# Performance work log

Measured on AMD Instinct MI355X. Metric: run time of the kernel, lower is better.

## Reference

```python
import jax, jax.numpy as jnp
import numpy as np

EMBED_DIM = 1024
NUM_HEADS = 16
HEAD_DIM = EMBED_DIM // NUM_HEADS


def setup_inputs() -> dict:
    key = jax.random.key(0)
    ks = jax.random.split(key, 9)
    B, T, D = 2, 4096, EMBED_DIM
    scale = 1.0 / np.sqrt(D)
    x = jax.random.normal(ks[0], (B, T, D), dtype=jnp.float32)
    # nn.Linear weights stored as (out, in); we use (in, out) layout via transpose-free init
    Wq = jax.random.uniform(ks[1], (D, D), dtype=jnp.float32, minval=-scale, maxval=scale)
    Wk = jax.random.uniform(ks[2], (D, D), dtype=jnp.float32, minval=-scale, maxval=scale)
    Wv = jax.random.uniform(ks[3], (D, D), dtype=jnp.float32, minval=-scale, maxval=scale)
    Wo = jax.random.uniform(ks[4], (D, D), dtype=jnp.float32, minval=-scale, maxval=scale)
    bq = jax.random.uniform(ks[5], (D,), dtype=jnp.float32, minval=-scale, maxval=scale)
    bk = jax.random.uniform(ks[6], (D,), dtype=jnp.float32, minval=-scale, maxval=scale)
    bv = jax.random.uniform(ks[7], (D,), dtype=jnp.float32, minval=-scale, maxval=scale)
    bo = jax.random.uniform(ks[8], (D,), dtype=jnp.float32, minval=-scale, maxval=scale)
    return {"x": x, "Wq": Wq, "bq": bq, "Wk": Wk, "bk": bk,
            "Wv": Wv, "bv": bv, "Wo": Wo, "bo": bo}


def reference(x, Wq, bq, Wk, bk, Wv, bv, Wo, bo):
    B, T, D = x.shape
    H, Hd = NUM_HEADS, HEAD_DIM
    q = x @ Wq + bq  # [B,T,D]
    k = x @ Wk + bk
    v = x @ Wv + bv
    # [B,T,D] -> [B,H,T,Hd]
    q = q.reshape(B, T, H, Hd).transpose(0, 2, 1, 3)
    k = k.reshape(B, T, H, Hd).transpose(0, 2, 1, 3)
    v = v.reshape(B, T, H, Hd).transpose(0, 2, 1, 3)
    att = jnp.einsum('bhqd,bhkd->bhqk', q, k) / jnp.sqrt(jnp.float32(Hd))
    causal = jnp.tril(jnp.ones((T, T), dtype=bool))  # True = keep
    att = jnp.where(causal, att, -jnp.inf)
    att = jax.nn.softmax(att, axis=-1)
    out = jnp.einsum('bhqk,bhkd->bhqd', att, v)  # [B,H,T,Hd]
    out = out.transpose(0, 2, 1, 3).reshape(B, T, D)
    return out @ Wo + bo
```

## Files before the change

### kernel.cpp

```cpp
#include <hip/hip_runtime.h>
#include <hip/hip_bf16.h>
#include <math.h>

typedef __bf16 bf16;
typedef __attribute__((ext_vector_type(8))) __bf16 bf16x8;
typedef __attribute__((ext_vector_type(4))) __bf16 bf16x4;
typedef __attribute__((ext_vector_type(4))) short short4v;
typedef __attribute__((ext_vector_type(4))) float f32x4;

#define MFMA16(a,b,c)  __builtin_amdgcn_mfma_f32_16x16x32_bf16((a),(b),(c),0,0,0)
#define MFMAK16(a,b,c) __builtin_amdgcn_mfma_f32_16x16x16bf16_1k((a),(b),(c),0,0,0)

__device__ __forceinline__ void gload16(const void* gp, void* lp) {
  __builtin_amdgcn_global_load_lds(
      (const __attribute__((address_space(1))) void*)gp,
      (__attribute__((address_space(3))) void*)lp, 16, 0, 0);
}

__global__ __launch_bounds__(256) void cast_x(
    const float* __restrict__ x, bf16* __restrict__ xb)
{
  size_t i = ((size_t)blockIdx.x*256 + threadIdx.x) * 8;
  f32x4 a = *(const f32x4*)(x+i);
  f32x4 b = *(const f32x4*)(x+i+4);
  bf16x8 o;
  #pragma unroll
  for (int j=0;j<4;j++) { o[j] = (bf16)a[j]; o[4+j] = (bf16)b[j]; }
  *(bf16x8*)(xb+i) = o;
}

__global__ __launch_bounds__(1024) void tr_cast(
    const float* __restrict__ w0, const float* __restrict__ w1,
    const float* __restrict__ w2, bf16* __restrict__ dst)
{
  __shared__ bf16 tile[64][65];
  const float* src = (blockIdx.z==0)?w0:(blockIdx.z==1)?w1:w2;
  bf16* d = dst + (size_t)blockIdx.z * (1024*1024);
  int x = threadIdx.x, y = threadIdx.y;
  int tc = blockIdx.x, tr = blockIdx.y;
  #pragma unroll
  for (int i=0;i<4;i++) {
    int r = y + i*16;
    tile[r][x] = (bf16)src[(size_t)(tr*64+r)*1024 + tc*64 + x];
  }
  __syncthreads();
  #pragma unroll
  for (int i=0;i<4;i++) {
    int r = y + i*16;
    d[(size_t)(tc*64+r)*1024 + tr*64 + x] = tile[x][r];
  }
}

__global__ __launch_bounds__(1024) void v_tr(
    const bf16* __restrict__ v, bf16* __restrict__ vt)
{
  __shared__ bf16 tile[64][65];
  int x = threadIdx.x, y = threadIdx.y;
  int tt = blockIdx.x;
  int bh = blockIdx.y;
  int b = bh >> 4, h = bh & 15;
  const bf16* src = v + ((size_t)b*4096 + tt*64)*1024 + h*64;
  bf16* dst = vt + ((size_t)bh*64)*4096 + tt*64;
  #pragma unroll
  for (int i=0;i<4;i++) {
    int r = y + i*16;
    tile[r][x] = src[(size_t)r*1024 + x];
  }
  __syncthreads();
  #pragma unroll
  for (int i=0;i<4;i++) {
    int r = y + i*16;
    dst[(size_t)r*4096 + x] = tile[x][r];
  }
}

__global__ __launch_bounds__(256) void gemm_qkv(
    const bf16* __restrict__ A, const bf16* __restrict__ Bt,
    const float* __restrict__ bq, const float* __restrict__ bk, const float* __restrict__ bv,
    bf16* __restrict__ q, bf16* __restrict__ k, bf16* __restrict__ v,
    int M, int K)
{
  __shared__ __align__(16) bf16 As[128*64];
  __shared__ __align__(16) bf16 Bs[128*64];
  const int tid  = threadIdx.x;
  const int wave = tid >> 6;
  const int lane = tid & 63;
  const int l15  = lane & 15;
  const int quad = lane >> 4;

  const int wg  = blockIdx.x + blockIdx.y*24;
  const int nid = (wg & 7)*192 + (wg >> 3);
  const int m0 = (nid / 24) * 128;
  const int n0 = (nid % 24) * 128;

  const int wm = (wave >> 1) * 64;
  const int wn = (wave & 1) * 64;

  int srow[4], scol[4];
  #pragma unroll
  for (int p=0;p<4;p++) {
    int cid = p*256 + tid;
    srow[p] = cid >> 3;
    scol[p] = ((cid & 7) ^ (srow[p] & 7)) << 3;
  }
  const int swz8 = l15 & 7;
  int rdo[2];
  #pragma unroll
  for (int kk=0;kk<2;kk++) rdo[kk] = (((kk*4 + quad) ^ swz8) << 3);

  f32x4 acc[4][4];
  #pragma unroll
  for (int i=0;i<4;i++)
    #pragma unroll
    for (int j=0;j<4;j++)
      acc[i][j] = (f32x4){0.f,0.f,0.f,0.f};

  for (int k0 = 0; k0 < K; k0 += 64) {
    __syncthreads();
    #pragma unroll
    for (int p=0;p<4;p++) {
      int cid = p*256 + tid;
      gload16(A  + (size_t)(m0+srow[p])*K + k0 + scol[p], As + cid*8);
      gload16(Bt + (size_t)(n0+srow[p])*K + k0 + scol[p], Bs + cid*8);
    }
    __syncthreads();
    #pragma unroll
    for (int kk=0;kk<2;kk++) {
      bf16x8 af[4], bfr[4];
      #pragma unroll
      for (int t=0;t<4;t++) {
        af[t]  = *(const bf16x8*)(As + (wm + t*16 + l15)*64 + rdo[kk]);
        bfr[t] = *(const bf16x8*)(Bs + (wn + t*16 + l15)*64 + rdo[kk]);
      }
      #pragma unroll
      for (int mt=0;mt<4;mt++)
        #pragma unroll
        for (int nt=0;nt<4;nt++)
          acc[mt][nt] = MFMA16(af[mt], bfr[nt], acc[mt][nt]);
    }
  }

  const int mat = n0 >> 10;
  const float* bsel = (mat==0) ? bq : (mat==1) ? bk : bv;
  bf16*       osel  = (mat==0) ? q  : (mat==1) ? k  : v;
  const float qsc   = (mat==0) ? 0.1803368801f : 1.0f;
  #pragma unroll
  for (int nt=0;nt<4;nt++) {
    int col = n0 + wn + nt*16 + l15;
    int cw  = col & 1023;
    float bvv = bsel[cw];
    #pragma unroll
    for (int mt=0;mt<4;mt++) {
      int row = m0 + wm + mt*16 + quad*4;
      #pragma unroll
      for (int r=0;r<4;r++)
        osel[(size_t)(row + r)*1024 + cw] = (bf16)((acc[mt][nt][r] + bvv) * qsc);
    }
  }
}

__global__ __launch_bounds__(256, 4) void gemm_out(
    const bf16* __restrict__ A, const bf16* __restrict__ Bt,
    const float* __restrict__ bias, float* __restrict__ C,
    int M, int N, int K)
{
  __shared__ __align__(16) bf16 As[128*64];
  __shared__ __align__(16) bf16 Bs[64*64];
  const int tid  = threadIdx.x;
  const int wave = tid >> 6;
  const int lane = tid & 63;
  const int l15  = lane & 15;
  const int quad = lane >> 4;

  const int wg  = blockIdx.x + blockIdx.y*16;
  const int nid = (wg & 7)*128 + (wg >> 3);
  const int m0 = (nid / 16) * 128;
  const int n0 = (nid % 16) * 64;

  const int wm = (wave >> 1) * 64;
  const int wn = (wave & 1) * 32;

  int srow[4], scol[4];
  #pragma unroll
  for (int p=0;p<4;p++) {
    int cid = p*256 + tid;
    srow[p] = cid >> 3;
    scol[p] = ((cid & 7) ^ (srow[p] & 7)) << 3;
  }
  const int swz8 = l15 & 7;
  int rdo[2];
  #pragma unroll
  for (int kk=0;kk<2;kk++) rdo[kk] = (((kk*4 + quad) ^ swz8) << 3);

  f32x4 acc[4][2];
  #pragma unroll
  for (int i=0;i<4;i++)
    #pragma unroll
    for (int j=0;j<2;j++)
      acc[i][j] = (f32x4){0.f,0.f,0.f,0.f};

  for (int k0 = 0; k0 < K; k0 += 64) {
    __syncthreads();
    #pragma unroll
    for (int p=0;p<4;p++)
      gload16(A + (size_t)(m0+srow[p])*K + k0 + scol[p], As + (p*256+tid)*8);
    #pragma unroll
    for (int p=0;p<2;p++) {
      int cid = p*256 + tid;
      gload16(Bt + (size_t)(n0+srow[p])*K + k0 + scol[p], Bs + cid*8);
    }
    __syncthreads();
    #pragma unroll
    for (int kk=0;kk<2;kk++) {
      bf16x8 af[4], bfr[2];
      #pragma unroll
      for (int t=0;t<4;t++)
        af[t]  = *(const bf16x8*)(As + (wm + t*16 + l15)*64 + rdo[kk]);
      #pragma unroll
      for (int t=0;t<2;t++)
        bfr[t] = *(const bf16x8*)(Bs + (wn + t*16 + l15)*64 + rdo[kk]);
      #pragma unroll
      for (int mt=0;mt<4;mt++)
        #pragma unroll
        for (int nt=0;nt<2;nt++)
          acc[mt][nt] = MFMA16(af[mt], bfr[nt], acc[mt][nt]);
    }
  }

  #pragma unroll
  for (int nt=0;nt<2;nt++) {
    int col = n0 + wn + nt*16 + l15;
    float bvv = bias[col];
    #pragma unroll
    for (int mt=0;mt<4;mt++) {
      int row = m0 + wm + mt*16 + quad*4;
      #pragma unroll
      for (int r=0;r<4;r++)
        C[(size_t)(row + r)*N + col] = acc[mt][nt][r] + bvv;
    }
  }
}

__global__ __launch_bounds__(256, 2) void attn_fwd(
    const bf16* __restrict__ Q, const bf16* __restrict__ Kp,
    const bf16* __restrict__ Vtg, bf16* __restrict__ O)
{
  __shared__ __align__(16) char KsB[4*8192];
  __shared__ __align__(16) char VtB[4*8192];

  const int tid  = threadIdx.x;
  const int w    = tid >> 6;
  const int lane = tid & 63;
  const int l15  = lane & 15;
  const int quad = lane >> 4;

  const int bid = blockIdx.x;
  const int pp  = bid >> 5;
  const int bh  = bid & 31;
  const int h   = bh & 15;
  const int b   = bh >> 4;

  const size_t headoff = (size_t)h * 64;
  const size_t bbase   = (size_t)b * 4096;

  short4v ones_s;
  {
    bf16x4 o1;
    #pragma unroll
    for (int j=0;j<4;j++) o1[j] = (bf16)1.0f;
    ones_s = __builtin_bit_cast(short4v, o1);
  }

  const int kt_row = tid >> 2;
  const int kswz   = (kt_row & 7) << 4;
  const int ks_w0  = kt_row*128 + (((tid & 3)*32)      ^ kswz);
  const int ks_w1  = kt_row*128 + (((tid & 3)*32 + 16) ^ kswz);

  const int vd  = tid >> 2;
  const int vt0 = (tid & 3) * 16;
  int vw[4];
  #pragma unroll
  for (int u=0;u<4;u++)
    vw[u] = vd*128 + (((vt0 + u*4)*2) ^ ((vd & 15) << 3));

  const int s7    = l15 & 7;
  const int ks_r0 = l15*128 + ((quad ^ (s7 & 3)) << 4) + ((s7 >> 2) << 6);
  const int ks_r1 = ks_r0 ^ 64;
  const int vt_rbase = l15*128 + ((quad ^ (l15 & 3)) << 3) + ((l15 >> 2) << 5);
  int vt_r[4];
  #pragma unroll
  for (int tt=0;tt<4;tt++) vt_r[tt] = vt_rbase ^ (tt << 5);

  const bf16* kbase0 = Kp  + (bbase + kt_row)*1024 + headoff + (tid & 3)*16;
  const bf16* vbase0 = Vtg + ((size_t)(bh*64) + vd)*4096 + vt0;

  for (int ph = 0; ph < 2; ++ph) {
    const int qt = ph ? (31 - pp) : pp;
    const int q0 = qt * 128;
    const int ktmax = 2*qt + 1;

    bf16x8 aqA[2], aqB[2];
    {
      int rowA = q0 + w*16 + l15;
      const bf16* qp = Q + (bbase + rowA)*1024 + headoff + quad*8;
      aqA[0] = *(const bf16x8*)(qp);
      aqA[1] = *(const bf16x8*)(qp + 32);
      qp += 64*1024;
      aqB[0] = *(const bf16x8*)(qp);
      aqB[1] = *(const bf16x8*)(qp + 32);
    }

    f32x4 accoA[4], accoB[4], accliA, accliB;
    #pragma unroll
    for (int i=0;i<4;i++) { accoA[i] = (f32x4){0.f,0.f,0.f,0.f}; accoB[i] = (f32x4){0.f,0.f,0.f,0.f}; }
    accliA = (f32x4){0.f,0.f,0.f,0.f};
    accliB = (f32x4){0.f,0.f,0.f,0.f};

    __syncthreads();
    #pragma unroll
    for (int j=0;j<2;j++) {
      const bf16* kp = kbase0 + (size_t)j*64*1024;
      const bf16* vp = vbase0 + j*64;
      bf16x8 k0 = *(const bf16x8*)(kp);
      bf16x8 k1 = *(const bf16x8*)(kp + 8);
      bf16x8 v0 = *(const bf16x8*)(vp);
      bf16x8 v1 = *(const bf16x8*)(vp + 8);
      char* ksn = KsB + j*8192;
      char* vtn = VtB + j*8192;
      *(bf16x8*)(ksn + ks_w0) = k0;
      *(bf16x8*)(ksn + ks_w1) = k1;
      *(bf16x4*)(vtn + vw[0]) = __builtin_shufflevector(v0, v0, 0,1,2,3);
      *(bf16x4*)(vtn + vw[1]) = __builtin_shufflevector(v0, v0, 4,5,6,7);
      *(bf16x4*)(vtn + vw[2]) = __builtin_shufflevector(v1, v1, 0,1,2,3);
      *(bf16x4*)(vtn + vw[3]) = __builtin_shufflevector(v1, v1, 4,5,6,7);
    }
    __syncthreads();

    const bf16* kpref = kbase0 + (size_t)2*64*1024;
    const bf16* vpref = vbase0 + 128;

    for (int kt = 0; kt <= ktmax; ++kt) {
      const bool pre = (kt + 2 <= ktmax);

      bf16x8 kr0, kr1, vr0, vr1;
      if (pre) {
        kr0 = *(const bf16x8*)(kpref);
        kr1 = *(const bf16x8*)(kpref + 8);
        vr0 = *(const bf16x8*)(vpref);
        vr1 = *(const bf16x8*)(vpref + 8);
        kpref += 64*1024;
        vpref += 64;
      }

      const char* ksb = KsB + (kt & 3)*8192;
      const char* vtb = VtB + (kt & 3)*8192;

      f32x4 accsA[4], accsB[4];
      #pragma unroll
      for (int i=0;i<4;i++) { accsA[i] = (f32x4){0.f,0.f,0.f,0.f}; accsB[i] = (f32x4){0.f,0.f,0.f,0.f}; }

      __builtin_amdgcn_s_setprio(1);
      #pragma unroll
      for (int kk=0;kk<2;kk++) {
        #pragma unroll
        for (int tt=0;tt<4;tt++) {
          bf16x8 ka = *(const bf16x8*)(ksb + (kk ? ks_r1 : ks_r0) + tt*2048);
          accsA[tt] = MFMA16(ka, aqA[kk], accsA[tt]);
          accsB[tt] = MFMA16(ka, aqB[kk], accsB[tt]);
        }
      }
      __builtin_amdgcn_s_setprio(0);

      short4v ptsA[4], ptsB[4];
      if (kt < 2*qt) {
        #pragma unroll
        for (int tt=0;tt<4;tt++) {
          bf16x4 pa, pb;
          #pragma unroll
          for (int r=0;r<4;r++) {
            pa[r] = (bf16)__builtin_amdgcn_exp2f(accsA[tt][r]);
            pb[r] = (bf16)__builtin_amdgcn_exp2f(accsB[tt][r]);
          }
          ptsA[tt] = __builtin_bit_cast(short4v, pa);
          ptsB[tt] = __builtin_bit_cast(short4v, pb);
        }
      } else {
        const bool adead = (kt > 2*qt);
        #pragma unroll
        for (int tt=0;tt<4;tt++) {
          bf16x4 pa, pb;
          #pragma unroll
          for (int r=0;r<4;r++) {
            const bool tq = (tt*16 + quad*4 + r > w*16 + l15);
            float fa = __builtin_amdgcn_exp2f(accsA[tt][r]);
            if (adead || tq) fa = 0.0f;
            float fb = __builtin_amdgcn_exp2f(accsB[tt][r]);
            if (adead && tq) fb = 0.0f;
            pa[r] = (bf16)fa; pb[r] = (bf16)fb;
          }
          ptsA[tt] = __builtin_bit_cast(short4v, pa);
          ptsB[tt] = __builtin_bit_cast(short4v, pb);
        }
      }

      __builtin_amdgcn_s_setprio(1);
      #pragma unroll
      for (int nt=0;nt<4;nt++) {
        #pragma unroll
        for (int tt=0;tt<4;tt++) {
          bf16x4 va = *(const bf16x4*)(vtb + vt_r[tt] + nt*2048);
          short4v vas = __builtin_bit_cast(short4v, va);
          accoA[nt] = MFMAK16(vas, ptsA[tt], accoA[nt]);
          accoB[nt] = MFMAK16(vas, ptsB[tt], accoB[nt]);
        }
      }
      #pragma unroll
      for (int tt=0;tt<4;tt++) {
        accliA = MFMAK16(ones_s, ptsA[tt], accliA);
        accliB = MFMAK16(ones_s, ptsB[tt], accliB);
      }
      __builtin_amdgcn_s_setprio(0);

      if (pre) {
        char* ksn = KsB + ((kt + 2) & 3)*8192;
        char* vtn = VtB + ((kt + 2) & 3)*8192;
        *(bf16x8*)(ksn + ks_w0) = kr0;
        *(bf16x8*)(ksn + ks_w1) = kr1;
        *(bf16x4*)(vtn + vw[0]) = __builtin_shufflevector(vr0, vr0, 0,1,2,3);
        *(bf16x4*)(vtn + vw[1]) = __builtin_shufflevector(vr0, vr0, 4,5,6,7);
        *(bf16x4*)(vtn + vw[2]) = __builtin_shufflevector(vr1, vr1, 0,1,2,3);
        *(bf16x4*)(vtn + vw[3]) = __builtin_shufflevector(vr1, vr1, 4,5,6,7);
      }
      if (kt & 1) __syncthreads();
    }

    {
      float invA = 1.0f / accliA[0];
      float invB = 1.0f / accliB[0];
      int rowA = q0 + w*16 + l15;
      bf16* obA = O + (bbase + rowA)*1024 + headoff;
      bf16* obB = obA + 64*1024;
      #pragma unroll
      for (int nt=0;nt<4;nt++) {
        bf16x4 oA, oB;
        #pragma unroll
        for (int r=0;r<4;r++) {
          oA[r] = (bf16)(accoA[nt][r] * invA);
          oB[r] = (bf16)(accoB[nt][r] * invB);
        }
        *(bf16x4*)(obA + nt*16 + quad*4) = oA;
        *(bf16x4*)(obB + nt*16 + quad*4) = oB;
      }
    }
  }
}

extern "C" void kernel_launch(void* const* d_in, const int* in_sizes, int n_in,
                              void* d_out, int out_size, void* d_ws, size_t ws_size,
                              hipStream_t stream) {
  const float* x  = (const float*)d_in[0];
  const float* Wq = (const float*)d_in[1];
  const float* bq = (const float*)d_in[2];
  const float* Wk = (const float*)d_in[3];
  const float* bk = (const float*)d_in[4];
  const float* Wv = (const float*)d_in[5];
  const float* bv = (const float*)d_in[6];
  const float* Wo = (const float*)d_in[7];
  const float* bo = (const float*)d_in[8];
  float* out = (float*)d_out;

  bf16* ws = (bf16*)d_ws;
  bf16* q  = ws;
  bf16* k  = q + (size_t)8192*1024;
  bf16* v  = k + (size_t)8192*1024;
  bf16* xb = v + (size_t)8192*1024;
  bf16* ao = q;
  bf16* WtQKV = (bf16*)d_out;
  bf16* vT    = (bf16*)d_out;
  bf16* WtO   = xb;

  tr_cast<<<dim3(16,16,3), dim3(64,16), 0, stream>>>(Wq, Wk, Wv, WtQKV);
  cast_x<<<4096, 256, 0, stream>>>(x, xb);
  gemm_qkv<<<dim3(24,64), 256, 0, stream>>>(xb, WtQKV, bq, bk, bv, q, k, v, 8192, 1024);
  v_tr<<<dim3(64,32), dim3(64,16), 0, stream>>>(v, vT);
  tr_cast<<<dim3(16,16,1), dim3(64,16), 0, stream>>>(Wo, Wo, Wo, WtO);
  attn_fwd<<<512, 256, 0, stream>>>(q, k, vT, ao);
  gemm_out<<<dim3(16,64), 256, 0, stream>>>(ao, WtO, bo, out, 8192, 1024, 1024);
}
```

Before: 296.2 us.

## Software-pipeline QK^T of next key tile with softmax/PV of current tile

Restructures the attention inner loop so the QK^T MFMAs for key tile kt+1 are issued before the exp/mask and PV work of tile kt. Two ping-pong score accumulator sets are used, and a macro unrolls the loop by two. The aim is to overlap the transcendental and conversion work with matrix-core work and shorten the dependency chain within each iteration. In exchange it holds an extra 32 floats of accumulator state, which risks register pressure under launch_bounds(256,2). It also adds a __syncthreads every iteration where there was one every other iteration.

```diff
diff --git a/kernel.cpp b/kernel.cpp
--- a/kernel.cpp
+++ b/kernel.cpp
@@ -241,6 +241,102 @@
   }
 }
 
+#define ATTN_ITER(CURA, CURB, NXTA, NXTB, KT)                                  \
+  {                                                                            \
+    const int kt_ = (KT);                                                      \
+    const bool pre_ = (kt_ + 2 <= ktmax);                                      \
+    bf16x8 kr0, kr1, vr0, vr1;                                                 \
+    if (pre_) {                                                                \
+      kr0 = *(const bf16x8*)(kpref);                                           \
+      kr1 = *(const bf16x8*)(kpref + 8);                                       \
+      vr0 = *(const bf16x8*)(vpref);                                           \
+      vr1 = *(const bf16x8*)(vpref + 8);                                       \
+      kpref += 64*1024;                                                        \
+      vpref += 64;                                                             \
+    }                                                                          \
+    if (kt_ < ktmax) {                                                         \
+      const char* ksb_ = KsB + ((kt_ + 1) & 3)*8192;                           \
+      _Pragma("unroll")                                                        \
+      for (int i=0;i<4;i++) {                                                  \
+        NXTA[i] = (f32x4){0.f,0.f,0.f,0.f};                                    \
+        NXTB[i] = (f32x4){0.f,0.f,0.f,0.f};                                    \
+      }                                                                        \
+      __builtin_amdgcn_s_setprio(1);                                           \
+      _Pragma("unroll")                                                        \
+      for (int kk=0;kk<2;kk++) {                                               \
+        _Pragma("unroll")                                                      \
+        for (int tt=0;tt<4;tt++) {                                             \
+          bf16x8 ka = *(const bf16x8*)(ksb_ + (kk ? ks_r1 : ks_r0) + tt*2048); \
+          NXTA[tt] = MFMA16(ka, aqA[kk], NXTA[tt]);                            \
+          NXTB[tt] = MFMA16(ka, aqB[kk], NXTB[tt]);                            \
+        }                                                                      \
+      }                                                                        \
+      __builtin_amdgcn_s_setprio(0);                                           \
+    }                                                                          \
+    short4v ptsA[4], ptsB[4];                                                  \
+    if (kt_ < qt2) {                                                           \
+      _Pragma("unroll")                                                        \
+      for (int tt=0;tt<4;tt++) {                                               \
+        bf16x4 pa, pb;                                                         \
+        _Pragma("unroll")                                                      \
+        for (int r=0;r<4;r++) {                                                \
+          pa[r] = (bf16)__builtin_amdgcn_exp2f(CURA[tt][r]);                   \
+          pb[r] = (bf16)__builtin_amdgcn_exp2f(CURB[tt][r]);                   \
+        }                                                                      \
+        ptsA[tt] = __builtin_bit_cast(short4v, pa);                            \
+        ptsB[tt] = __builtin_bit_cast(short4v, pb);                            \
+      }                                                                        \
+    } else {                                                                   \
+      const bool adead = (kt_ > qt2);                                          \
+      _Pragma("unroll")                                                        \
+      for (int tt=0;tt<4;tt++) {                                               \
+        bf16x4 pa, pb;                                                         \
+        _Pragma("unroll")                                                      \
+        for (int r=0;r<4;r++) {                                                \
+          const bool tq = (tt*16 + quad*4 + r > w*16 + l15);                   \
+          float fa = __builtin_amdgcn_exp2f(CURA[tt][r]);                      \
+          if (adead || tq) fa = 0.0f;                                          \
+          float fb = __builtin_amdgcn_exp2f(CURB[tt][r]);                      \
+          if (adead && tq) fb = 0.0f;                                          \
+          pa[r] = (bf16)fa; pb[r] = (bf16)fb;                                  \
+        }                                                                      \
+        ptsA[tt] = __builtin_bit_cast(short4v, pa);                            \
+        ptsB[tt] = __builtin_bit_cast(short4v, pb);                            \
+      }                                                                        \
+    }                                                                          \
+    {                                                                          \
+      const char* vtb_ = VtB + (kt_ & 3)*8192;                                 \
+      __builtin_amdgcn_s_setprio(1);                                           \
+      _Pragma("unroll")                                                        \
+      for (int nt=0;nt<4;nt++) {                                               \
+        _Pragma("unroll")                                                      \
+        for (int tt=0;tt<4;tt++) {                                             \
+          bf16x4 va = *(const bf16x4*)(vtb_ + vt_r[tt] + nt*2048);             \
+          short4v vas = __builtin_bit_cast(short4v, va);                       \
+          accoA[nt] = MFMAK16(vas, ptsA[tt], accoA[nt]);                       \
+          accoB[nt] = MFMAK16(vas, ptsB[tt], accoB[nt]);                       \
+        }                                                                      \
+      }                                                                        \
+      _Pragma("unroll")                                                        \
+      for (int tt=0;tt<4;tt++) {                                               \
+        accliA = MFMAK16(ones_s, ptsA[tt], accliA);                            \
+        accliB = MFMAK16(ones_s, ptsB[tt], accliB);                            \
+      }                                                                        \
+      __builtin_amdgcn_s_setprio(0);                                           \
+    }                                                                          \
+    if (pre_) {                                                                \
+      char* ksn = KsB + ((kt_ + 2) & 3)*8192;                                  \
+      char* vtn = VtB + ((kt_ + 2) & 3)*8192;                                  \
+      *(bf16x8*)(ksn + ks_w0) = kr0;                                           \
+      *(bf16x8*)(ksn + ks_w1) = kr1;                                           \
+      *(bf16x4*)(vtn + vw[0]) = __builtin_shufflevector(vr0, vr0, 0,1,2,3);    \
+      *(bf16x4*)(vtn + vw[1]) = __builtin_shufflevector(vr0, vr0, 4,5,6,7);    \
+      *(bf16x4*)(vtn + vw[2]) = __builtin_shufflevector(vr1, vr1, 0,1,2,3);    \
+      *(bf16x4*)(vtn + vw[3]) = __builtin_shufflevector(vr1, vr1, 4,5,6,7);    \
+    }                                                                          \
+    __syncthreads();                                                           \
+  }
+
 __global__ __launch_bounds__(256, 2) void attn_fwd(
     const bf16* __restrict__ Q, const bf16* __restrict__ Kp,
     const bf16* __restrict__ Vtg, bf16* __restrict__ O)
@@ -298,6 +394,7 @@
     const int qt = ph ? (31 - pp) : pp;
     const int q0 = qt * 128;
     const int ktmax = 2*qt + 1;
+    const int qt2   = 2*qt;
 
     bf16x8 aqA[2], aqB[2];
     {
@@ -339,99 +436,26 @@
     const bf16* kpref = kbase0 + (size_t)2*64*1024;
     const bf16* vpref = vbase0 + 128;
 
-    for (int kt = 0; kt <= ktmax; ++kt) {
-      const bool pre = (kt + 2 <= ktmax);
-
-      bf16x8 kr0, kr1, vr0, vr1;
-      if (pre) {
-        kr0 = *(const bf16x8*)(kpref);
-        kr1 = *(const bf16x8*)(kpref + 8);
-        vr0 = *(const bf16x8*)(vpref);
-        vr1 = *(const bf16x8*)(vpref + 8);
-        kpref += 64*1024;
-        vpref += 64;
-      }
-
-      const char* ksb = KsB + (kt & 3)*8192;
-      const char* vtb = VtB + (kt & 3)*8192;
-
-      f32x4 accsA[4], accsB[4];
-      #pragma unroll
-      for (int i=0;i<4;i++) { accsA[i] = (f32x4){0.f,0.f,0.f,0.f}; accsB[i] = (f32x4){0.f,0.f,0.f,0.f}; }
-
+    f32x4 c0A[4], c0B[4], c1A[4], c1B[4];
+    #pragma unroll
+    for (int i=0;i<4;i++) { c0A[i] = (f32x4){0.f,0.f,0.f,0.f}; c0B[i] = (f32x4){0.f,0.f,0.f,0.f}; }
+    {
       __builtin_amdgcn_s_setprio(1);
       #pragma unroll
       for (int kk=0;kk<2;kk++) {
         #pragma unroll
         for (int tt=0;tt<4;tt++) {
-          bf16x8 ka = *(const bf16x8*)(ksb + (kk ? ks_r1 : ks_r0) + tt*2048);
-          accsA[tt] = MFMA16(ka, aqA[kk], accsA[tt]);
-          accsB[tt] = MFMA16(ka, aqB[kk], accsB[tt]);
+          bf16x8 ka = *(const bf16x8*)(KsB + (kk ? ks_r1 : ks_r0) + tt*2048);
+          c0A[tt] = MFMA16(ka, aqA[kk], c0A[tt]);
+          c0B[tt] = MFMA16(ka, aqB[kk], c0B[tt]);
         }
       }
       __builtin_amdgcn_s_setprio(0);
-
-      short4v ptsA[4], ptsB[4];
-      if (kt < 2*qt) {
-        #pragma unroll
-        for (int tt=0;tt<4;tt++) {
-          bf16x4 pa, pb;
-          #pragma unroll
-          for (int r=0;r<4;r++) {
-            pa[r] = (bf16)__builtin_amdgcn_exp2f(accsA[tt][r]);
-            pb[r] = (bf16)__builtin_amdgcn_exp2f(accsB[tt][r]);
-          }
-          ptsA[tt] = __builtin_bit_cast(short4v, pa);
-          ptsB[tt] = __builtin_bit_cast(short4v, pb);
-        }
-      } else {
-        const bool adead = (kt > 2*qt);
-        #pragma unroll
-        for (int tt=0;tt<4;tt++) {
-          bf16x4 pa, pb;
-          #pragma unroll
-          for (int r=0;r<4;r++) {
-            const bool tq = (tt*16 + quad*4 + r > w*16 + l15);
-            float fa = __builtin_amdgcn_exp2f(accsA[tt][r]);
-            if (adead || tq) fa = 0.0f;
-            float fb = __builtin_amdgcn_exp2f(accsB[tt][r]);
-            if (adead && tq) fb = 0.0f;
-            pa[r] = (bf16)fa; pb[r] = (bf16)fb;
-          }
-          ptsA[tt] = __builtin_bit_cast(short4v, pa);
-          ptsB[tt] = __builtin_bit_cast(short4v, pb);
-        }
-      }
-
-      __builtin_amdgcn_s_setprio(1);
-      #pragma unroll
-      for (int nt=0;nt<4;nt++) {
-        #pragma unroll
-        for (int tt=0;tt<4;tt++) {
-          bf16x4 va = *(const bf16x4*)(vtb + vt_r[tt] + nt*2048);
-          short4v vas = __builtin_bit_cast(short4v, va);
-          accoA[nt] = MFMAK16(vas, ptsA[tt], accoA[nt]);
-          accoB[nt] = MFMAK16(vas, ptsB[tt], accoB[nt]);
-        }
-      }
-      #pragma unroll
-      for (int tt=0;tt<4;tt++) {
-        accliA = MFMAK16(ones_s, ptsA[tt], accliA);
-        accliB = MFMAK16(ones_s, ptsB[tt], accliB);
-      }
-      __builtin_amdgcn_s_setprio(0);
-
-      if (pre) {
-        char* ksn = KsB + ((kt + 2) & 3)*8192;
-        char* vtn = VtB + ((kt + 2) & 3)*8192;
-        *(bf16x8*)(ksn + ks_w0) = kr0;
-        *(bf16x8*)(ksn + ks_w1) = kr1;
-        *(bf16x4*)(vtn + vw[0]) = __builtin_shufflevector(vr0, vr0, 0,1,2,3);
-        *(bf16x4*)(vtn + vw[1]) = __builtin_shufflevector(vr0, vr0, 4,5,6,7);
-        *(bf16x4*)(vtn + vw[2]) = __builtin_shufflevector(vr1, vr1, 0,1,2,3);
-        *(bf16x4*)(vtn + vw[3]) = __builtin_shufflevector(vr1, vr1, 4,5,6,7);
-      }
-      if (kt & 1) __syncthreads();
+    }
+
+    for (int kt = 0; kt <= ktmax; kt += 2) {
+      ATTN_ITER(c0A, c0B, c1A, c1B, kt);
+      ATTN_ITER(c1A, c1B, c0A, c0B, kt + 1);
     }
 
     {
```

Measured after the change: 309.7 us. 1.05x slower.
